# Optimization experiments

Measured on AMD Instinct MI355X. Metric: run time of the kernel, lower is better.

## Reference

```python
import jax, jax.numpy as jnp
import numpy as np

B, S, E, H, L, V = 4, 1024, 256, 512, 16, 8000


def setup_inputs() -> dict:
    key = jax.random.key(0)
    ks = jax.random.split(key, 8)
    return {
        "sent": jax.random.randint(ks[0], (B, S), 0, V),
        "mask": jax.random.randint(ks[1], (B, S), 0, 2),
        "char_emb_w": jax.random.normal(ks[2], (V, E), dtype=jnp.float32) * 0.02,
        "mask_emb_w": jax.random.normal(ks[3], (2, E), dtype=jnp.float32) * 0.02,
        "wA": jax.random.normal(ks[4], (E, H), dtype=jnp.float32) * (1.0 / np.sqrt(E)),
        "bA": jnp.zeros((H,), dtype=jnp.float32),
        "wB": jax.random.normal(ks[5], (E, H), dtype=jnp.float32) * (1.0 / np.sqrt(E)),
        "bB": jnp.zeros((H,), dtype=jnp.float32),
        "wS": jax.random.normal(ks[6], (E, L), dtype=jnp.float32) * (1.0 / np.sqrt(E)),
        "bS": jnp.zeros((L,), dtype=jnp.float32),
    }


def reference(sent, mask, char_emb_w, mask_emb_w, wA, bA, wB, bB, wS, bS):
    # Embedding lookups: (B,S,E)
    ce = char_emb_w[sent]
    me = mask_emb_w[mask]
    # vemb = char_emb * GELU(mask_emb)  (torch GELU default = exact erf form)
    vemb = ce * jax.nn.gelu(me, approximate=False)
    va = vemb @ wA + bA                      # (B,S,H)
    vb = jax.nn.sigmoid(vemb @ wB + bB)      # (B,S,H)
    vc = jnp.einsum("bih,bjh->bij", va, vb) / H   # (B,S,S), biaffine score
    vd = jax.nn.relu(vemb @ wS + bS)         # (B,S,L)
    # torch: matmul(vc.unsqueeze(3), vd.unsqueeze(2)) -> (B,S,S,L) rank-1 outer product
    pred = jax.nn.softmax(vc[..., None] * vd[:, :, None, :], axis=-1)
    return pred
```

## Files before the change

### kernel.cpp

```cpp
#include <hip/hip_runtime.h>
#include <hip/hip_bf16.h>
#include <math.h>

typedef __attribute__((ext_vector_type(8))) short short8;
typedef __attribute__((ext_vector_type(4))) float f32x4;
typedef unsigned short u16;

#define Sn 1024
#define En 256
#define Hn 512
#define Ln 16

__device__ inline u16 bf16b(float x) {
    union { __hip_bfloat16 h; u16 u; } cvt;
    cvt.h = __float2bfloat16(x);
    return cvt.u;
}

__global__ void prep_embed(const float* __restrict__ wA, const float* __restrict__ wB,
                           const float* __restrict__ wS, u16* __restrict__ Wt,
                           const int* __restrict__ sent, const int* __restrict__ mask,
                           const float* __restrict__ ce_w, const float* __restrict__ me_w,
                           u16* __restrict__ vemb) {
    int bx = blockIdx.x;
    if (bx < 1088) {
        int idx = bx * 256 + threadIdx.x;
        int n = idx >> 8;
        int k = idx & 255;
        float v = 0.f;
        if (n < 512)       v = wA[k * 512 + n];
        else if (n < 1024) v = wB[k * 512 + (n - 512)];
        else if (n < 1040) v = wS[k * 16 + (n - 1024)];
        Wt[idx] = bf16b(v);
    } else {
        int row = bx - 1088;
        int e = threadIdx.x;
        int s = sent[row];
        int m = mask[row];
        float ce = ce_w[s * En + e];
        float me = me_w[m * En + e];
        float g = 0.5f * me * (1.f + erff(me * 0.70710678118654752f));
        vemb[row * En + e] = bf16b(ce * g);
    }
}

#define LDP 136
__global__ __launch_bounds__(256, 2) void gemm1(const u16* __restrict__ A, const u16* __restrict__ Bt,
                                                const float* __restrict__ bA, const float* __restrict__ bB,
                                                const float* __restrict__ bS,
                                                u16* __restrict__ va, u16* __restrict__ vb,
                                                float* __restrict__ vd,
                                                float* __restrict__ dmn, float* __restrict__ dmx) {
    __shared__ __align__(16) u16 As[64 * LDP];
    __shared__ __align__(16) u16 Bs[64 * LDP];
    int tid = threadIdx.x;
    int m0 = blockIdx.x * 64, n0 = blockIdx.y * 64;
    int lane = tid & 63, w = tid >> 6;
    int lrow = lane & 15, quad = lane >> 4;

    f32x4 acc[4];
    for (int nt = 0; nt < 4; nt++) acc[nt] = (f32x4){0.f, 0.f, 0.f, 0.f};

    for (int kb = 0; kb < 2; kb++) {
        for (int i = 0; i < 4; i++) {
            int off = (i * 256 + tid) * 8;
            int r = off >> 7, c = off & 127;
            *(short8*)&As[r * LDP + c] = *(const short8*)&A[(m0 + r) * 256 + kb * 128 + c];
            *(short8*)&Bs[r * LDP + c] = *(const short8*)&Bt[(n0 + r) * 256 + kb * 128 + c];
        }
        __syncthreads();
        for (int ks = 0; ks < 4; ks++) {
            short8 a = *(const short8*)&As[(w * 16 + lrow) * LDP + ks * 32 + quad * 8];
            for (int nt = 0; nt < 4; nt++) {
                short8 b = *(const short8*)&Bs[(nt * 16 + lrow) * LDP + ks * 32 + quad * 8];
                acc[nt] = __builtin_amdgcn_mfma_f32_16x16x32_bf16(a, b, acc[nt], 0, 0, 0);
            }
        }
        __syncthreads();
    }
    int mbase = m0 + w * 16 + quad * 4;
    if (blockIdx.y < 8) {
        for (int nt = 0; nt < 4; nt++) {
            int n = n0 + nt * 16 + lrow;
            float bias = bA[n];
            for (int r = 0; r < 4; r++)
                va[(mbase + r) * 512 + n] = bf16b(acc[nt][r] + bias);
        }
    } else if (blockIdx.y < 16) {
        for (int nt = 0; nt < 4; nt++) {
            int n = n0 + nt * 16 + lrow - 512;
            float bias = bB[n];
            for (int r = 0; r < 4; r++) {
                float x = acc[nt][r] + bias;
                vb[(mbase + r) * 512 + n] = bf16b(1.f / (1.f + __expf(-x)));
            }
        }
    } else {
        float bias = bS[lrow];
        for (int r = 0; r < 4; r++) {
            float x = acc[0][r] + bias;
            x = x > 0.f ? x : 0.f;
            vd[(mbase + r) * 16 + lrow] = x;
            float mn = x, mx = x;
            for (int d = 1; d < 16; d <<= 1) {
                mn = fminf(mn, __shfl_xor(mn, d));
                mx = fmaxf(mx, __shfl_xor(mx, d));
            }
            if (lrow == 0) {
                dmn[mbase + r] = mn;
                dmx[mbase + r] = mx;
            }
        }
    }
}

__global__ __launch_bounds__(256, 2) void gemm2_softmax(const u16* __restrict__ va_g,
                                                        const u16* __restrict__ vb_g,
                                                        const float* __restrict__ vd,
                                                        const float* __restrict__ dmn,
                                                        const float* __restrict__ dmx,
                                                        float* __restrict__ out) {
    __shared__ __align__(16) u16 As[64 * LDP];
    __shared__ __align__(16) u16 Bs[64 * LDP];
    int tid = threadIdx.x;
    int b = blockIdx.z;
    int m0 = blockIdx.x * 64, n0 = blockIdx.y * 64;
    const u16* A  = va_g + (size_t)b * 1024 * 512;
    const u16* Bt = vb_g + (size_t)b * 1024 * 512;
    int lane = tid & 63, w = tid >> 6;
    int lrow = lane & 15, quad = lane >> 4;

    f32x4 acc[4];
    for (int nt = 0; nt < 4; nt++) acc[nt] = (f32x4){0.f, 0.f, 0.f, 0.f};

    for (int kb = 0; kb < 4; kb++) {
        for (int i = 0; i < 4; i++) {
            int off = (i * 256 + tid) * 8;
            int r = off >> 7, c = off & 127;
            *(short8*)&As[r * LDP + c] = *(const short8*)&A[(m0 + r) * 512 + kb * 128 + c];
            *(short8*)&Bs[r * LDP + c] = *(const short8*)&Bt[(n0 + r) * 512 + kb * 128 + c];
        }
        __syncthreads();
        for (int ks = 0; ks < 4; ks++) {
            short8 a = *(const short8*)&As[(w * 16 + lrow) * LDP + ks * 32 + quad * 8];
            for (int nt = 0; nt < 4; nt++) {
                short8 bfr = *(const short8*)&Bs[(nt * 16 + lrow) * LDP + ks * 32 + quad * 8];
                acc[nt] = __builtin_amdgcn_mfma_f32_16x16x32_bf16(a, bfr, acc[nt], 0, 0, 0);
            }
        }
        __syncthreads();
    }

    const float invH = 1.0f / 512.0f;
    int mbase = m0 + w * 16 + quad * 4;
    for (int nt = 0; nt < 4; nt++) {
        int n = n0 + nt * 16 + lrow;
        int rowd = b * 1024 + n;
        float4 d0 = *(const float4*)&vd[rowd * 16 + 0];
        float4 d1 = *(const float4*)&vd[rowd * 16 + 4];
        float4 d2 = *(const float4*)&vd[rowd * 16 + 8];
        float4 d3 = *(const float4*)&vd[rowd * 16 + 12];
        float mn = dmn[rowd], mx = dmx[rowd];
        for (int r = 0; r < 4; r++) {
            float c = acc[nt][r] * invH;
            float m = (c >= 0.f) ? c * mx : c * mn;
            float e[16];
            e[0]  = __expf(c * d0.x - m); e[1]  = __expf(c * d0.y - m);
            e[2]  = __expf(c * d0.z - m); e[3]  = __expf(c * d0.w - m);
            e[4]  = __expf(c * d1.x - m); e[5]  = __expf(c * d1.y - m);
            e[6]  = __expf(c * d1.z - m); e[7]  = __expf(c * d1.w - m);
            e[8]  = __expf(c * d2.x - m); e[9]  = __expf(c * d2.y - m);
            e[10] = __expf(c * d2.z - m); e[11] = __expf(c * d2.w - m);
            e[12] = __expf(c * d3.x - m); e[13] = __expf(c * d3.y - m);
            e[14] = __expf(c * d3.z - m); e[15] = __expf(c * d3.w - m);
            float s = 0.f;
            for (int l = 0; l < 16; l++) s += e[l];
            float inv = 1.f / s;
            size_t base = (((size_t)(b * 1024 + mbase + r)) * 1024 + n) * 16;
            float4 o;
            o.x = e[0] * inv;  o.y = e[1] * inv;  o.z = e[2] * inv;  o.w = e[3] * inv;
            *(float4*)&out[base + 0] = o;
            o.x = e[4] * inv;  o.y = e[5] * inv;  o.z = e[6] * inv;  o.w = e[7] * inv;
            *(float4*)&out[base + 4] = o;
            o.x = e[8] * inv;  o.y = e[9] * inv;  o.z = e[10] * inv; o.w = e[11] * inv;
            *(float4*)&out[base + 8] = o;
            o.x = e[12] * inv; o.y = e[13] * inv; o.z = e[14] * inv; o.w = e[15] * inv;
            *(float4*)&out[base + 12] = o;
        }
    }
}

extern "C" void kernel_launch(void* const* d_in, const int* in_sizes, int n_in,
                              void* d_out, int out_size, void* d_ws, size_t ws_size,
                              hipStream_t stream) {
    const int*   sent = (const int*)d_in[0];
    const int*   mask = (const int*)d_in[1];
    const float* ce_w = (const float*)d_in[2];
    const float* me_w = (const float*)d_in[3];
    const float* wA   = (const float*)d_in[4];
    const float* bA   = (const float*)d_in[5];
    const float* wB   = (const float*)d_in[6];
    const float* bB   = (const float*)d_in[7];
    const float* wS   = (const float*)d_in[8];
    const float* bS   = (const float*)d_in[9];
    float* out = (float*)d_out;

    char* ws = (char*)d_ws;
    u16* vemb = (u16*)ws;  ws += (size_t)4096 * 256 * 2;
    u16* Wt   = (u16*)ws;  ws += (size_t)1088 * 256 * 2;
    u16* va   = (u16*)ws;  ws += (size_t)4096 * 512 * 2;
    u16* vb   = (u16*)ws;  ws += (size_t)4096 * 512 * 2;
    float* vd  = (float*)ws;  ws += (size_t)4096 * 16 * 4;
    float* dmn = (float*)ws;  ws += (size_t)4096 * 4;
    float* dmx = (float*)ws;  ws += (size_t)4096 * 4;

    prep_embed<<<5184, 256, 0, stream>>>(wA, wB, wS, Wt, sent, mask, ce_w, me_w, vemb);
    gemm1<<<dim3(64, 17), 256, 0, stream>>>(vemb, Wt, bA, bB, bS, va, vb, vd, dmn, dmx);
    gemm2_softmax<<<dim3(16, 16, 4), 256, 0, stream>>>(va, vb, vd, dmn, dmx, out);
}
```

Before: 353.6 us.

## Split biaffine GEMM and softmax expansion into separate kernels via vc buffer

Unfuses the softmax epilogue from the biaffine GEMM. The GEMM now writes the scaled score matrix to a 16 MB workspace, and a new elementwise kernel has four threads per (i,j) pair compute the 16-way softmax, writing coalesced nontemporal float4 stores. The goal is to make the dominant 256 MB output write fully coalesced and not limited by GEMM occupancy. The cost is an extra write and read of the vc buffer plus one more kernel launch.

```diff
diff --git a/kernel.cpp b/kernel.cpp
--- a/kernel.cpp
+++ b/kernel.cpp
@@ -114,12 +114,8 @@
     }
 }
 
-__global__ __launch_bounds__(256, 2) void gemm2_softmax(const u16* __restrict__ va_g,
-                                                        const u16* __restrict__ vb_g,
-                                                        const float* __restrict__ vd,
-                                                        const float* __restrict__ dmn,
-                                                        const float* __restrict__ dmx,
-                                                        float* __restrict__ out) {
+__global__ __launch_bounds__(256, 2) void gemm2(const u16* __restrict__ va_g, const u16* __restrict__ vb_g,
+                                                float* __restrict__ vc) {
     __shared__ __align__(16) u16 As[64 * LDP];
     __shared__ __align__(16) u16 Bs[64 * LDP];
     int tid = threadIdx.x;
@@ -150,44 +146,40 @@
         }
         __syncthreads();
     }
-
     const float invH = 1.0f / 512.0f;
+    float* C = vc + (size_t)b * 1024 * 1024;
     int mbase = m0 + w * 16 + quad * 4;
     for (int nt = 0; nt < 4; nt++) {
         int n = n0 + nt * 16 + lrow;
-        int rowd = b * 1024 + n;
-        float4 d0 = *(const float4*)&vd[rowd * 16 + 0];
-        float4 d1 = *(const float4*)&vd[rowd * 16 + 4];
-        float4 d2 = *(const float4*)&vd[rowd * 16 + 8];
-        float4 d3 = *(const float4*)&vd[rowd * 16 + 12];
-        float mn = dmn[rowd], mx = dmx[rowd];
-        for (int r = 0; r < 4; r++) {
-            float c = acc[nt][r] * invH;
-            float m = (c >= 0.f) ? c * mx : c * mn;
-            float e[16];
-            e[0]  = __expf(c * d0.x - m); e[1]  = __expf(c * d0.y - m);
-            e[2]  = __expf(c * d0.z - m); e[3]  = __expf(c * d0.w - m);
-            e[4]  = __expf(c * d1.x - m); e[5]  = __expf(c * d1.y - m);
-            e[6]  = __expf(c * d1.z - m); e[7]  = __expf(c * d1.w - m);
-            e[8]  = __expf(c * d2.x - m); e[9]  = __expf(c * d2.y - m);
-            e[10] = __expf(c * d2.z - m); e[11] = __expf(c * d2.w - m);
-            e[12] = __expf(c * d3.x - m); e[13] = __expf(c * d3.y - m);
-            e[14] = __expf(c * d3.z - m); e[15] = __expf(c * d3.w - m);
-            float s = 0.f;
-            for (int l = 0; l < 16; l++) s += e[l];
-            float inv = 1.f / s;
-            size_t base = (((size_t)(b * 1024 + mbase + r)) * 1024 + n) * 16;
-            float4 o;
-            o.x = e[0] * inv;  o.y = e[1] * inv;  o.z = e[2] * inv;  o.w = e[3] * inv;
-            *(float4*)&out[base + 0] = o;
-            o.x = e[4] * inv;  o.y = e[5] * inv;  o.z = e[6] * inv;  o.w = e[7] * inv;
-            *(float4*)&out[base + 4] = o;
-            o.x = e[8] * inv;  o.y = e[9] * inv;  o.z = e[10] * inv; o.w = e[11] * inv;
-            *(float4*)&out[base + 8] = o;
-            o.x = e[12] * inv; o.y = e[13] * inv; o.z = e[14] * inv; o.w = e[15] * inv;
-            *(float4*)&out[base + 12] = o;
-        }
-    }
+        for (int r = 0; r < 4; r++)
+            C[(mbase + r) * 1024 + n] = acc[nt][r] * invH;
+    }
+}
+
+__global__ __launch_bounds__(256) void expand(const float* __restrict__ vc, const float* __restrict__ vd,
+                                              const float* __restrict__ dmn, const float* __restrict__ dmx,
+                                              float* __restrict__ out) {
+    int gid = blockIdx.x * 256 + threadIdx.x;
+    int t = gid & 3;
+    int grp = gid >> 2;
+    int j = grp & 1023;
+    int bi = grp >> 10;
+    int b = bi >> 10;
+    float c = __builtin_nontemporal_load(&vc[grp]);
+    int rowd = b * 1024 + j;
+    f32x4 d = *(const f32x4*)&vd[rowd * 16 + t * 4];
+    float m = (c >= 0.f) ? c * dmx[rowd] : c * dmn[rowd];
+    float e0 = __expf(c * d.x - m);
+    float e1 = __expf(c * d.y - m);
+    float e2 = __expf(c * d.z - m);
+    float e3 = __expf(c * d.w - m);
+    float s = e0 + e1 + e2 + e3;
+    s += __shfl_xor(s, 1);
+    s += __shfl_xor(s, 2);
+    float inv = 1.f / s;
+    f32x4 o;
+    o.x = e0 * inv; o.y = e1 * inv; o.z = e2 * inv; o.w = e3 * inv;
+    __builtin_nontemporal_store(o, (f32x4*)&out[(size_t)grp * 16 + t * 4]);
 }
 
 extern "C" void kernel_launch(void* const* d_in, const int* in_sizes, int n_in,
@@ -213,8 +205,10 @@
     float* vd  = (float*)ws;  ws += (size_t)4096 * 16 * 4;
     float* dmn = (float*)ws;  ws += (size_t)4096 * 4;
     float* dmx = (float*)ws;  ws += (size_t)4096 * 4;
+    float* vc  = (float*)ws;  ws += (size_t)4 * 1024 * 1024 * 4;
 
     prep_embed<<<5184, 256, 0, stream>>>(wA, wB, wS, Wt, sent, mask, ce_w, me_w, vemb);
     gemm1<<<dim3(64, 17), 256, 0, stream>>>(vemb, Wt, bA, bB, bS, va, vb, vd, dmn, dmx);
-    gemm2_softmax<<<dim3(16, 16, 4), 256, 0, stream>>>(va, vb, vd, dmn, dmx, out);
-}
+    gemm2<<<dim3(16, 16, 4), 256, 0, stream>>>(va, vb, vc);
+    expand<<<65536, 256, 0, stream>>>(vc, vd, dmn, dmx, out);
+}
```

Result: faster. 306.3 us, median of 2 (-13.4%).
